# Optimization experiments

Measured on AMD Instinct MI355X. Metric: run time of the kernel, lower is better.

The kernel has to match this reference:

```python
import jax, jax.numpy as jnp
import numpy as np
import math

B, LQ, S, D = 8, 4096, 77, 1024
H, HD = 16, 64
R, ALPHA = 192, 16.0
LORA_SCALE = ALPHA / R
N_SUBJ = 32


def setup_inputs() -> dict:
    key = jax.random.key(0)
    ks = jax.random.split(key, 16)
    w = 0.02
    return {
        "hidden_states": jax.random.normal(ks[0], (B, LQ, D), jnp.float32),
        "encoder_hidden_states": jax.random.normal(ks[1], (B, S, D), jnp.float32),
        "Wq": jax.random.normal(ks[2], (D, D), jnp.float32) * w,
        "Wk": jax.random.normal(ks[3], (D, D), jnp.float32) * w,
        "Wv": jax.random.normal(ks[4], (D, D), jnp.float32) * w,
        "Wo": jax.random.normal(ks[5], (D, D), jnp.float32) * w,
        "bo": jnp.zeros((D,), jnp.float32),
        "Ak": jax.random.normal(ks[6], (R, D), jnp.float32) * w,
        "Bk": jax.random.normal(ks[7], (D, R), jnp.float32) * w,
        "Av": jax.random.normal(ks[8], (R, D), jnp.float32) * w,
        "Bv": jax.random.normal(ks[9], (D, R), jnp.float32) * w,
        "Ao": jax.random.normal(ks[10], (R, D), jnp.float32) * w,
        "Bo": jax.random.normal(ks[11], (D, R), jnp.float32) * w,
        "cross_attn_scale_factor": jnp.ones((), jnp.float32),
        "subj_b": jax.random.randint(ks[12], (N_SUBJ,), 0, B, jnp.int32),
        "subj_n": jax.random.randint(ks[13], (N_SUBJ,), 0, S, jnp.int32),
    }


def _lora(x, A, Bm):
    # peft LoRA delta: scale * (x @ A^T) @ B^T
    return LORA_SCALE * ((x @ A.T) @ Bm.T)


def reference(hidden_states, encoder_hidden_states, Wq, Wk, Wv, Wo, bo,
              Ak, Bk, Av, Bv, Ao, Bo, cross_attn_scale_factor, subj_b, subj_n):
    hs, ehs = hidden_states, encoder_hidden_states
    # q_lora_updates_query=False -> query uses the base projection only
    q = hs @ Wq.T                                  # [B, LQ, D]
    k = ehs @ Wk.T + _lora(ehs, Ak, Bk)            # [B, S, D] (to_k_lora)
    v = ehs @ Wv.T + _lora(ehs, Av, Bv)            # [B, S, D] (to_v_lora)

    q = q.reshape(B, LQ, H, HD).transpose(0, 2, 1, 3)   # [B,H,LQ,HD]
    k = k.reshape(B, S, H, HD).transpose(0, 2, 1, 3)    # [B,H,S,HD]
    v = v.reshape(B, S, H, HD).transpose(0, 2, 1, 3)

    scale = 1.0 / math.sqrt(HD)
    attn_score = jnp.einsum('bhld,bhsd->bhls', q, k) * scale  # [B,H,LQ,S]

    # normalize_cross_attn: zero-center subject-token scores over query dim,
    # then rescale by the learned cross_attn_scale_factor.
    sub = attn_score[subj_b, :, :, subj_n]                    # [K,H,LQ]
    sub = (sub - sub.mean(axis=2, keepdims=True)) * cross_attn_scale_factor
    attn_score = attn_score.at[subj_b, :, :, subj_n].set(sub)

    attn_weight = jax.nn.softmax(attn_score, axis=-1)
    out = jnp.einsum('bhls,bhsd->bhld', attn_weight, v)       # [B,H,LQ,HD]
    out = out.transpose(0, 2, 1, 3).reshape(B, LQ, D)

    # to_out_lora: base out-proj (with bias) + LoRA delta; to_out[1] dropout = id
    out = out @ Wo.T + bo + _lora(out, Ao, Bo)
    return out
```

## Files before the change

kernel.cpp:

```cpp
#include <hip/hip_runtime.h>
#include <stdint.h>

#define B_     8
#define LQ_    4096
#define S_     77
#define SP_    80
#define D_     1024
#define H_     16
#define HD_    64
#define NC_    1280
#define NSUBJ_ 32

typedef __attribute__((ext_vector_type(4))) float  f4;
typedef __attribute__((ext_vector_type(8))) short  short8;
typedef __attribute__((ext_vector_type(8))) unsigned short us8;
typedef __attribute__((ext_vector_type(4))) unsigned short us4;

__device__ __forceinline__ unsigned short f2bf(float f) {
  union { float f; unsigned u; } x; x.f = f;
  unsigned r = x.u + 0x7FFFu + ((x.u >> 16) & 1u);
  return (unsigned short)(r >> 16);
}

__device__ __forceinline__ void gload16(const void* g, void* s) {
  __builtin_amdgcn_global_load_lds((const __attribute__((address_space(1))) void*)g,
                                   (__attribute__((address_space(3))) void*)s, 16, 0, 0);
}

__global__ __launch_bounds__(256) void k_hssum(const float* __restrict__ hs,
                                               float* __restrict__ part,
                                               unsigned short* __restrict__ hsb) {
  int b = blockIdx.y;
  size_t base = ((size_t)b * LQ_ + (size_t)blockIdx.x * 64) * D_ + threadIdx.x * 4;
  f4 acc = {0.f, 0.f, 0.f, 0.f};
  for (int l = 0; l < 64; ++l) {
    f4 v = *(const f4*)(hs + base + (size_t)l * D_);
    acc += v;
    if (hsb) {
      us4 o;
#pragma unroll
      for (int j = 0; j < 4; ++j) o[j] = f2bf(v[j]);
      *(us4*)(hsb + base + (size_t)l * D_) = o;
    }
  }
  *(f4*)(part + (size_t)blockIdx.x * (B_ * D_) + b * D_ + threadIdx.x * 4) = acc;
}

__global__ __launch_bounds__(256) void k_hsred(const float* __restrict__ part,
                                               float* __restrict__ hssum) {
  int i = blockIdx.x * 256 + threadIdx.x;
  float s = 0.f;
  for (int x = 0; x < 64; ++x) s += part[(size_t)x * (B_ * D_) + i];
  hssum[i] = s;
}

__global__ __launch_bounds__(256) void k_tr4(const float* __restrict__ Wq, const float* __restrict__ Ak,
                                             const float* __restrict__ Av, const float* __restrict__ Ao,
                                             float* __restrict__ wqT, float* __restrict__ akT,
                                             float* __restrict__ avT, float* __restrict__ aoT) {
  int z = blockIdx.z;
  const float* in = z == 0 ? Wq : (z == 1 ? Ak : (z == 2 ? Av : Ao));
  float* out = z == 0 ? wqT : (z == 1 ? akT : (z == 2 ? avT : aoT));
  int R = z == 0 ? 1024 : 192;
  const int C = 1024;
  int c0 = blockIdx.x * 32, r0 = blockIdx.y * 32;
  if (r0 >= R) return;
  __shared__ float tile[32][33];
  int tx = threadIdx.x & 31, ty = threadIdx.x >> 5;
#pragma unroll
  for (int k = 0; k < 4; ++k)
    tile[ty + 8 * k][tx] = in[(size_t)(r0 + ty + 8 * k) * C + c0 + tx];
  __syncthreads();
#pragma unroll
  for (int k = 0; k < 4; ++k)
    out[(size_t)(c0 + ty + 8 * k) * R + r0 + tx] = tile[tx][ty + 8 * k];
}

template <bool OBF>
__device__ __forceinline__ void gemm64_body(
    const float* __restrict__ A, int lda, const float* __restrict__ Bt, int ldb,
    void* __restrict__ Cv, int ldc, long cbase, const float* __restrict__ Dm, int ldd,
    int M, int Mv, int N, int K, float alpha, int m0, int n0,
    short* As, short* Bs) {
  int t = threadIdx.x, lane = t & 63, wid = t >> 6;
  int wm = wid >> 1, wn = wid & 1;
  f4 acc[2][2] = {};
  int srow = t >> 2, skc = (t & 3) * 8;
  for (int k0 = 0; k0 < K; k0 += 32) {
    __syncthreads();
    f4 a0 = {0,0,0,0}, a1 = {0,0,0,0}, b0 = {0,0,0,0}, b1 = {0,0,0,0};
    if (m0 + srow < Mv) {
      const float* p = A + (size_t)(m0 + srow) * lda + k0 + skc;
      a0 = *(const f4*)p; a1 = *(const f4*)(p + 4);
    }
    if (n0 + srow < N) {
      const float* p = Bt + (size_t)(n0 + srow) * ldb + k0 + skc;
      b0 = *(const f4*)p; b1 = *(const f4*)(p + 4);
    }
    us8 ua, ub;
#pragma unroll
    for (int j = 0; j < 4; ++j) {
      ua[j] = f2bf(a0[j]); ua[4 + j] = f2bf(a1[j]);
      ub[j] = f2bf(b0[j]); ub[4 + j] = f2bf(b1[j]);
    }
    *(us8*)(As + srow * 40 + skc) = ua;
    *(us8*)(Bs + srow * 40 + skc) = ub;
    __syncthreads();
    short8 fa[2], fb[2];
#pragma unroll
    for (int i = 0; i < 2; ++i) {
      fa[i] = *(const short8*)(As + (wm * 32 + i * 16 + (lane & 15)) * 40 + (lane >> 4) * 8);
      fb[i] = *(const short8*)(Bs + (wn * 32 + i * 16 + (lane & 15)) * 40 + (lane >> 4) * 8);
    }
#pragma unroll
    for (int mi = 0; mi < 2; ++mi)
#pragma unroll
      for (int ni = 0; ni < 2; ++ni)
        acc[mi][ni] = __builtin_amdgcn_mfma_f32_16x16x32_bf16(fa[mi], fb[ni], acc[mi][ni], 0, 0, 0);
  }
#pragma unroll
  for (int mi = 0; mi < 2; ++mi)
#pragma unroll
    for (int ni = 0; ni < 2; ++ni)
#pragma unroll
      for (int j = 0; j < 4; ++j) {
        int row = m0 + wm * 32 + mi * 16 + (lane >> 4) * 4 + j;
        int col = n0 + wn * 32 + ni * 16 + (lane & 15);
        if (row < M && col < N) {
          float val = acc[mi][ni][j] * alpha;
          if (Dm) val += Dm[(size_t)row * ldd + col];
          size_t idx = (size_t)cbase + (size_t)row * ldc + col;
          if (OBF) ((unsigned short*)Cv)[idx] = f2bf(val);
          else     ((float*)Cv)[idx] = val;
        }
      }
}

template <bool OBF>
__global__ __launch_bounds__(256) void k_gemm_small(
    const float* __restrict__ A, int lda, long sA1, long sA2,
    const float* __restrict__ Bt, int ldb, long sB1, long sB2,
    void* __restrict__ Cv, int ldc, long sC1, long sC2,
    const float* __restrict__ Dm, int ldd,
    int M, int Mv, int N, int K, float alpha, int Z2) {
  int z = blockIdx.z, z1 = z / Z2, z2 = z - z1 * Z2;
  __shared__ short As[64 * 40];
  __shared__ short Bs[64 * 40];
  gemm64_body<OBF>(A + z1 * sA1 + z2 * sA2, lda, Bt + z1 * sB1 + z2 * sB2, ldb,
                   Cv, ldc, z1 * sC1 + z2 * sC2, Dm, ldd, M, Mv, N, K, alpha,
                   blockIdx.x * 64, blockIdx.y * 64, As, Bs);
}

__global__ __launch_bounds__(256) void k_weff(
    const float* __restrict__ Bk, const float* __restrict__ Bv, const float* __restrict__ Bo,
    const float* __restrict__ akT, const float* __restrict__ avT, const float* __restrict__ aoT,
    const float* __restrict__ Wk, const float* __restrict__ Wv, const float* __restrict__ Wo,
    float* __restrict__ weff, float alpha) {
  int z = blockIdx.z;
  const float* A  = z == 0 ? Bk : (z == 1 ? Bv : Bo);
  const float* Bt = z == 0 ? akT : (z == 1 ? avT : aoT);
  const float* Dm = z == 0 ? Wk : (z == 1 ? Wv : Wo);
  __shared__ short As[64 * 40];
  __shared__ short Bs[64 * 40];
  gemm64_body<false>(A, 192, Bt, 192, weff + (size_t)z * 1048576, 1024, 0, Dm, 1024,
                     1024, 1024, 1024, 192, alpha, blockIdx.x * 64, blockIdx.y * 64, As, Bs);
}

__global__ void k_mubeta(const float* __restrict__ hssum, const float* __restrict__ Wq,
                         const float* __restrict__ kv,
                         const int* __restrict__ sb, const int* __restrict__ sn,
                         const float* __restrict__ csf_p,
                         float* __restrict__ alphav, float* __restrict__ betav) {
  int h = blockIdx.x, b = blockIdx.y;
  int t = threadIdx.x;
  __shared__ float qp[64];
  {
    int hd = t >> 1, half = t & 1;
    const float* wr = Wq + (size_t)(h * 64 + hd) * D_ + half * 512;
    const float* hp = hssum + b * D_ + half * 512;
    float s = 0.f;
    for (int d = 0; d < 512; d += 4) {
      f4 w = *(const f4*)(wr + d);
      f4 x = *(const f4*)(hp + d);
      s += w[0] * x[0] + w[1] * x[1] + w[2] * x[2] + w[3] * x[3];
    }
    s += __shfl_xor(s, 1, 64);
    if (half == 0) qp[hd] = s * (1.f / 4096.f);
  }
  __syncthreads();
  int s = t;
  if (s >= SP_) return;
  const float* kp = kv + ((size_t)(b * SP_ + s)) * 2048 + h * HD_;
  float mu = 0.f;
#pragma unroll 8
  for (int hd = 0; hd < HD_; ++hd) mu += qp[hd] * kp[hd];
  mu *= 0.125f;
  bool subj = false;
  for (int i = 0; i < NSUBJ_; ++i) subj = subj || (sb[i] == b && sn[i] == s);
  float csf = *csf_p;
  int c = b * NC_ + h * SP_ + s;
  alphav[c] = subj ? csf : 1.f;
  betav[c] = (s >= S_) ? -1e30f : (subj ? -mu * csf : 0.f);
}

__global__ __launch_bounds__(512, 2) void k_score_big(
    const unsigned short* __restrict__ hsb, const unsigned short* __restrict__ Mt,
    const float* __restrict__ alphav, const float* __restrict__ betav,
    unsigned short* __restrict__ P) {
  extern __shared__ short lds[];
  const int ASZ = 256 * 64;
  const int BSZ = 320 * 64;
  int id = blockIdx.x;
  int x = id & 7, idp = id >> 3;
  int nt = idp & 3;
  int pid = (idp >> 2) * 8 + x;
  int b = pid >> 4, mt = pid & 15;
  int m0 = mt * 256, n0 = nt * 320;

  const unsigned short* Ab = hsb + (size_t)b * LQ_ * D_;
  const unsigned short* Bb = Mt + (size_t)b * NC_ * D_;
  const float* alp = alphav + b * NC_;
  const float* bet = betav + b * NC_;
  unsigned short* Pb = P + (size_t)b * LQ_ * NC_;

  int t = threadIdx.x, lane = t & 63, wid = t >> 6;
  int wm = wid >> 2, wn = wid & 3;
  int r = lane & 15, q = lane >> 4;
  f4 acc[8][5] = {};

  auto SA = [&](int bf, int k0, int p) {
    int cb = p * 512 + wid * 64;
    int cc = cb + lane;
    int row = cc >> 3, col = ((cc & 7) ^ (row & 7)) * 8;
    gload16(Ab + (size_t)(m0 + row) * D_ + k0 + col, (char*)(lds + bf * ASZ) + cb * 16);
  };
  auto SB = [&](int bf, int k0, int p) {
    int cb = p * 512 + wid * 64;
    int cc = cb + lane;
    int row = cc >> 3, col = ((cc & 7) ^ (row & 7)) * 8;
    gload16(Bb + (size_t)(n0 + row) * D_ + k0 + col, (char*)(lds + 2 * ASZ + bf * BSZ) + cb * 16);
  };

#pragma unroll
  for (int p = 0; p < 4; ++p) SA(0, 0, p);
#pragma unroll
  for (int p = 0; p < 5; ++p) SB(0, 0, p);

  for (int kt = 0; kt < 16; ++kt) {
    int cur = kt & 1;
    const short* Ar = lds + cur * ASZ;
    const short* Br = lds + 2 * ASZ + cur * BSZ;
    int k1 = (kt + 1) * 64;
    bool pre = kt < 15;
    int co0 = (q ^ (lane & 7)) * 8;
    int co1 = ((4 + q) ^ (lane & 7)) * 8;
    short8 fb[5], fa[4];

    if (pre) {
      SA(cur ^ 1, k1, 0); SA(cur ^ 1, k1, 1); SA(cur ^ 1, k1, 2); SA(cur ^ 1, k1, 3);
      SB(cur ^ 1, k1, 0);
      asm volatile("s_waitcnt vmcnt(5)" ::: "memory");
    } else {
      asm volatile("s_waitcnt vmcnt(0)" ::: "memory");
    }
    __builtin_amdgcn_s_barrier();
#pragma unroll
    for (int ni = 0; ni < 5; ++ni) fb[ni] = *(const short8*)(Br + (wn * 80 + ni * 16 + r) * 64 + co0);
#pragma unroll
    for (int mi = 0; mi < 4; ++mi) fa[mi] = *(const short8*)(Ar + (wm * 128 + mi * 16 + r) * 64 + co0);
    __builtin_amdgcn_s_setprio(1);
#pragma unroll
    for (int mi = 0; mi < 4; ++mi)
#pragma unroll
      for (int ni = 0; ni < 5; ++ni)
        acc[mi][ni] = __builtin_amdgcn_mfma_f32_16x16x32_bf16(fa[mi], fb[ni], acc[mi][ni], 0, 0, 0);
    __builtin_amdgcn_s_setprio(0);
    __builtin_amdgcn_s_barrier();

#pragma unroll
    for (int mi = 0; mi < 4; ++mi) fa[mi] = *(const short8*)(Ar + (wm * 128 + (4 + mi) * 16 + r) * 64 + co0);
    if (pre) { SB(cur ^ 1, k1, 1); SB(cur ^ 1, k1, 2); SB(cur ^ 1, k1, 3); SB(cur ^ 1, k1, 4); }
    __builtin_amdgcn_s_barrier();
    __builtin_amdgcn_s_setprio(1);
#pragma unroll
    for (int mi = 0; mi < 4; ++mi)
#pragma unroll
      for (int ni = 0; ni < 5; ++ni)
        acc[4 + mi][ni] = __builtin_amdgcn_mfma_f32_16x16x32_bf16(fa[mi], fb[ni], acc[4 + mi][ni], 0, 0, 0);
    __builtin_amdgcn_s_setprio(0);
    __builtin_amdgcn_s_barrier();

#pragma unroll
    for (int ni = 0; ni < 5; ++ni) fb[ni] = *(const short8*)(Br + (wn * 80 + ni * 16 + r) * 64 + co1);
#pragma unroll
    for (int mi = 0; mi < 4; ++mi) fa[mi] = *(const short8*)(Ar + (wm * 128 + mi * 16 + r) * 64 + co1);
    __builtin_amdgcn_s_barrier();
    __builtin_amdgcn_s_setprio(1);
#pragma unroll
    for (int mi = 0; mi < 4; ++mi)
#pragma unroll
      for (int ni = 0; ni < 5; ++ni)
        acc[mi][ni] = __builtin_amdgcn_mfma_f32_16x16x32_bf16(fa[mi], fb[ni], acc[mi][ni], 0, 0, 0);
    __builtin_amdgcn_s_setprio(0);
    __builtin_amdgcn_s_barrier();

#pragma unroll
    for (int mi = 0; mi < 4; ++mi) fa[mi] = *(const short8*)(Ar + (wm * 128 + (4 + mi) * 16 + r) * 64 + co1);
    __builtin_amdgcn_s_barrier();
    __builtin_amdgcn_s_setprio(1);
#pragma unroll
    for (int mi = 0; mi < 4; ++mi)
#pragma unroll
      for (int ni = 0; ni < 5; ++ni)
        acc[4 + mi][ni] = __builtin_amdgcn_mfma_f32_16x16x32_bf16(fa[mi], fb[ni], acc[4 + mi][ni], 0, 0, 0);
    __builtin_amdgcn_s_setprio(0);
    __builtin_amdgcn_s_barrier();
  }

  float al[5], be[5];
#pragma unroll
  for (int ni = 0; ni < 5; ++ni) {
    int cc = n0 + wn * 80 + ni * 16 + (lane & 15);
    al[ni] = alp[cc]; be[ni] = bet[cc];
  }
#pragma unroll
  for (int mi = 0; mi < 8; ++mi) {
#pragma unroll
    for (int j = 0; j < 4; ++j) {
      float v[5];
      float m = -3.0e38f;
#pragma unroll
      for (int ni = 0; ni < 5; ++ni) { v[ni] = acc[mi][ni][j] * al[ni] + be[ni]; m = fmaxf(m, v[ni]); }
#pragma unroll
      for (int off = 1; off < 16; off <<= 1) m = fmaxf(m, __shfl_xor(m, off, 64));
      float ssum = 0.f;
#pragma unroll
      for (int ni = 0; ni < 5; ++ni) { v[ni] = __expf(v[ni] - m); ssum += v[ni]; }
#pragma unroll
      for (int off = 1; off < 16; off <<= 1) ssum += __shfl_xor(ssum, off, 64);
      float inv = 1.f / ssum;
      int row = m0 + wm * 128 + mi * 16 + (lane >> 4) * 4 + j;
      size_t rb = (size_t)row * NC_ + n0 + wn * 80 + (lane & 15);
#pragma unroll
      for (int ni = 0; ni < 5; ++ni)
        Pb[rb + ni * 16] = f2bf(v[ni] * inv);
    }
  }
}

__global__ __launch_bounds__(256) void k_score_f32(
    const float* __restrict__ hs, const unsigned short* __restrict__ Mt,
    const float* __restrict__ alphav, const float* __restrict__ betav,
    unsigned short* __restrict__ P) {
  int id = blockIdx.x;
  int x = id & 7, idp = id >> 3;
  int n_t = idp & 7;
  int pid = (idp >> 3) * 8 + x;
  int b = pid >> 5, m_t = pid & 31;
  int m0 = m_t * 128, n0 = n_t * 160;
  const float* Af = hs + (size_t)b * LQ_ * D_;
  const unsigned short* Bb = Mt + (size_t)b * NC_ * D_;
  const float* alp = alphav + b * NC_;
  const float* bet = betav + b * NC_;
  unsigned short* Pb = P + (size_t)b * LQ_ * NC_;
  __shared__ short As[128 * 64];
  __shared__ short Bs[160 * 64];
  int t = threadIdx.x, lane = t & 63, wid = t >> 6;
  int wm = wid >> 1, wn = wid & 1;
  int srow = lane >> 3;
  int schunk = (lane & 7) ^ srow;
  f4 acc[4][5] = {};
  for (int k0 = 0; k0 < D_; k0 += 64) {
    __syncthreads();
    for (int i = wid; i < 20; i += 4)
      gload16(Bb + (size_t)(n0 + i * 8 + srow) * D_ + k0 + schunk * 8, (char*)Bs + i * 1024);
    int arow = t >> 3, ac = t & 7;
    int awc = ac ^ (arow & 7);
#pragma unroll
    for (int p = 0; p < 4; ++p) {
      int row = p * 32 + arow;
      const float* src = Af + (size_t)(m0 + row) * D_ + k0 + ac * 8;
      f4 v0 = *(const f4*)src;
      f4 v1 = *(const f4*)(src + 4);
      us8 u;
#pragma unroll
      for (int j = 0; j < 4; ++j) { u[j] = f2bf(v0[j]); u[4 + j] = f2bf(v1[j]); }
      *(us8*)(As + row * 64 + awc * 8) = u;
    }
    __syncthreads();
#pragma unroll
    for (int kk = 0; kk < 2; ++kk) {
      int co = ((kk * 4 + (lane >> 4)) ^ (lane & 7)) * 8;
      short8 fa[4], fb[5];
#pragma unroll
      for (int mi = 0; mi < 4; ++mi)
        fa[mi] = *(const short8*)(As + (wm * 64 + mi * 16 + (lane & 15)) * 64 + co);
#pragma unroll
      for (int ni = 0; ni < 5; ++ni)
        fb[ni] = *(const short8*)(Bs + (wn * 80 + ni * 16 + (lane & 15)) * 64 + co);
#pragma unroll
      for (int mi = 0; mi < 4; ++mi)
#pragma unroll
        for (int ni = 0; ni < 5; ++ni)
          acc[mi][ni] = __builtin_amdgcn_mfma_f32_16x16x32_bf16(fa[mi], fb[ni], acc[mi][ni], 0, 0, 0);
    }
  }
  float al[5], be[5];
#pragma unroll
  for (int ni = 0; ni < 5; ++ni) {
    int cc = n0 + wn * 80 + ni * 16 + (lane & 15);
    al[ni] = alp[cc]; be[ni] = bet[cc];
  }
#pragma unroll
  for (int mi = 0; mi < 4; ++mi) {
#pragma unroll
    for (int j = 0; j < 4; ++j) {
      float v[5];
      float m = -3.0e38f;
#pragma unroll
      for (int ni = 0; ni < 5; ++ni) { v[ni] = acc[mi][ni][j] * al[ni] + be[ni]; m = fmaxf(m, v[ni]); }
#pragma unroll
      for (int off = 1; off < 16; off <<= 1) m = fmaxf(m, __shfl_xor(m, off, 64));
      float ssum = 0.f;
#pragma unroll
      for (int ni = 0; ni < 5; ++ni) { v[ni] = __expf(v[ni] - m); ssum += v[ni]; }
#pragma unroll
      for (int off = 1; off < 16; off <<= 1) ssum += __shfl_xor(ssum, off, 64);
      float inv = 1.f / ssum;
      int row = m0 + wm * 64 + mi * 16 + (lane >> 4) * 4 + j;
      size_t rb = (size_t)row * NC_ + n0 + wn * 80 + (lane & 15);
#pragma unroll
      for (int ni = 0; ni < 5; ++ni)
        Pb[rb + ni * 16] = f2bf(v[ni] * inv);
    }
  }
}

__global__ __launch_bounds__(512, 2) void k_out_big(
    const unsigned short* __restrict__ P, const unsigned short* __restrict__ Ut,
    const float* __restrict__ bo, float* __restrict__ out) {
  extern __shared__ short lds[];
  const int ASZ = 256 * 64;
  int id = blockIdx.x;
  int x = id & 7, idp = id >> 3;
  int nt = idp & 3;
  int pid = (idp >> 2) * 8 + x;
  int b = pid >> 4, mt = pid & 15;
  int m0 = mt * 256, n0 = nt * 256;

  const unsigned short* Ab = P + (size_t)b * LQ_ * NC_;
  const unsigned short* Bb = Ut + (size_t)b * D_ * NC_;
  float* ob = out + (size_t)b * LQ_ * D_;

  int t = threadIdx.x, lane = t & 63, wid = t >> 6;
  int wm = wid >> 2, wn = wid & 3;
  int r = lane & 15, q = lane >> 4;
  f4 acc[8][4] = {};
  const int T = NC_ / 64;

  auto SA = [&](int bf, int k0, int p) {
    int cb = p * 512 + wid * 64;
    int cc = cb + lane;
    int row = cc >> 3, col = ((cc & 7) ^ (row & 7)) * 8;
    gload16(Ab + (size_t)(m0 + row) * NC_ + k0 + col, (char*)(lds + bf * ASZ) + cb * 16);
  };
  auto SB = [&](int bf, int k0, int p) {
    int cb = p * 512 + wid * 64;
    int cc = cb + lane;
    int row = cc >> 3, col = ((cc & 7) ^ (row & 7)) * 8;
    gload16(Bb + (size_t)(n0 + row) * NC_ + k0 + col, (char*)(lds + 2 * ASZ + bf * ASZ) + cb * 16);
  };

#pragma unroll
  for (int p = 0; p < 4; ++p) SA(0, 0, p);
#pragma unroll
  for (int p = 0; p < 4; ++p) SB(0, 0, p);

  for (int kt = 0; kt < T; ++kt) {
    int cur = kt & 1;
    const short* Ar = lds + cur * ASZ;
    const short* Br = lds + 2 * ASZ + cur * ASZ;
    int k1 = (kt + 1) * 64;
    bool pre = kt + 1 < T;
    int co0 = (q ^ (lane & 7)) * 8;
    int co1 = ((4 + q) ^ (lane & 7)) * 8;
    short8 fb[4], fa[4];

    if (pre) {
      SA(cur ^ 1, k1, 0); SA(cur ^ 1, k1, 1); SA(cur ^ 1, k1, 2); SA(cur ^ 1, k1, 3);
      asm volatile("s_waitcnt vmcnt(4)" ::: "memory");
    } else {
      asm volatile("s_waitcnt vmcnt(0)" ::: "memory");
    }
    __builtin_amdgcn_s_barrier();
#pragma unroll
    for (int ni = 0; ni < 4; ++ni) fb[ni] = *(const short8*)(Br + (wn * 64 + ni * 16 + r) * 64 + co0);
#pragma unroll
    for (int mi = 0; mi < 4; ++mi) fa[mi] = *(const short8*)(Ar + (wm * 128 + mi * 16 + r) * 64 + co0);
    __builtin_amdgcn_s_setprio(1);
#pragma unroll
    for (int mi = 0; mi < 4; ++mi)
#pragma unroll
      for (int ni = 0; ni < 4; ++ni)
        acc[mi][ni] = __builtin_amdgcn_mfma_f32_16x16x32_bf16(fa[mi], fb[ni], acc[mi][ni], 0, 0, 0);
    __builtin_amdgcn_s_setprio(0);
    __builtin_amdgcn_s_barrier();

#pragma unroll
    for (int mi = 0; mi < 4; ++mi) fa[mi] = *(const short8*)(Ar + (wm * 128 + (4 + mi) * 16 + r) * 64 + co0);
    if (pre) { SB(cur ^ 1, k1, 0); SB(cur ^ 1, k1, 1); SB(cur ^ 1, k1, 2); SB(cur ^ 1, k1, 3); }
    __builtin_amdgcn_s_barrier();
    __builtin_amdgcn_s_setprio(1);
#pragma unroll
    for (int mi = 0; mi < 4; ++mi)
#pragma unroll
      for (int ni = 0; ni < 4; ++ni)
        acc[4 + mi][ni] = __builtin_amdgcn_mfma_f32_16x16x32_bf16(fa[mi], fb[ni], acc[4 + mi][ni], 0, 0, 0);
    __builtin_amdgcn_s_setprio(0);
    __builtin_amdgcn_s_barrier();

#pragma unroll
    for (int ni = 0; ni < 4; ++ni) fb[ni] = *(const short8*)(Br + (wn * 64 + ni * 16 + r) * 64 + co1);
#pragma unroll
    for (int mi = 0; mi < 4; ++mi) fa[mi] = *(const short8*)(Ar + (wm * 128 + mi * 16 + r) * 64 + co1);
    __builtin_amdgcn_s_barrier();
    __builtin_amdgcn_s_setprio(1);
#pragma unroll
    for (int mi = 0; mi < 4; ++mi)
#pragma unroll
      for (int ni = 0; ni < 4; ++ni)
        acc[mi][ni] = __builtin_amdgcn_mfma_f32_16x16x32_bf16(fa[mi], fb[ni], acc[mi][ni], 0, 0, 0);
    __builtin_amdgcn_s_setprio(0);
    __builtin_amdgcn_s_barrier();

#pragma unroll
    for (int mi = 0; mi < 4; ++mi) fa[mi] = *(const short8*)(Ar + (wm * 128 + (4 + mi) * 16 + r) * 64 + co1);
    __builtin_amdgcn_s_barrier();
    __builtin_amdgcn_s_setprio(1);
#pragma unroll
    for (int mi = 0; mi < 4; ++mi)
#pragma unroll
      for (int ni = 0; ni < 4; ++ni)
        acc[4 + mi][ni] = __builtin_amdgcn_mfma_f32_16x16x32_bf16(fa[mi], fb[ni], acc[4 + mi][ni], 0, 0, 0);
    __builtin_amdgcn_s_setprio(0);
    __builtin_amdgcn_s_barrier();
  }

#pragma unroll
  for (int ni = 0; ni < 4; ++ni) {
    int col = n0 + wn * 64 + ni * 16 + (lane & 15);
    float bov = bo[col];
#pragma unroll
    for (int mi = 0; mi < 8; ++mi)
#pragma unroll
      for (int j = 0; j < 4; ++j) {
        int row = m0 + wm * 128 + mi * 16 + (lane >> 4) * 4 + j;
        ob[(size_t)row * D_ + col] = acc[mi][ni][j] + bov;
      }
  }
}

extern "C" void kernel_launch(void* const* d_in, const int* in_sizes, int n_in,
                              void* d_out, int out_size, void* d_ws, size_t ws_size,
                              hipStream_t stream) {
  const float* hs  = (const float*)d_in[0];
  const float* ehs = (const float*)d_in[1];
  const float* Wq  = (const float*)d_in[2];
  const float* Wk  = (const float*)d_in[3];
  const float* Wv  = (const float*)d_in[4];
  const float* Wo  = (const float*)d_in[5];
  const float* bo  = (const float*)d_in[6];
  const float* Ak  = (const float*)d_in[7];
  const float* Bk  = (const float*)d_in[8];
  const float* Av  = (const float*)d_in[9];
  const float* Bv  = (const float*)d_in[10];
  const float* Ao  = (const float*)d_in[11];
  const float* Bo  = (const float*)d_in[12];
  const float* csf = (const float*)d_in[13];
  const int*   sb  = (const int*)d_in[14];
  const int*   sn  = (const int*)d_in[15];
  float* out = (float*)d_out;

  hipFuncSetAttribute(reinterpret_cast<const void*>(k_score_big),
                      hipFuncAttributeMaxDynamicSharedMemorySize, 147456);
  hipFuncSetAttribute(reinterpret_cast<const void*>(k_out_big),
                      hipFuncAttributeMaxDynamicSharedMemorySize, 131072);

  char* ws = (char*)d_ws;
  unsigned short* P  = (unsigned short*)ws;
  unsigned short* Mt = (unsigned short*)(ws + 83886080);
  unsigned short* Ut = (unsigned short*)(ws + 104857600);
  const size_t NEED_HSB = 125829120ULL + 67108864ULL + 81920ULL;
  bool useHsb = ws_size >= NEED_HSB;
  unsigned short* hsb = useHsb ? (unsigned short*)(ws + 125829120) : nullptr;
  char* tail = useHsb ? (ws + 192937984) : (ws + 125829120);
  float* alphav = (float*)tail;
  float* betav  = (float*)(tail + 40960);
  float* kvbuf = (float*)(ws + 0);
  float* weff  = (float*)(ws + 5242880);
  float* wqT   = (float*)(ws + 17825792);
  float* aT    = (float*)(ws + 22020096);
  float* part  = (float*)(ws + 24379392);
  float* hssum = (float*)(ws + 26476544);

  float* woE = weff + 2097152;
  float* akT = aT;
  float* avT = aT + 196608;
  float* aoT = aT + 393216;

  const float LS = 16.0f / 192.0f;

  k_hssum<<<dim3(64, 8), 256, 0, stream>>>(hs, part, hsb);
  k_hsred<<<32, 256, 0, stream>>>(part, hssum);

  k_tr4<<<dim3(32, 32, 4), 256, 0, stream>>>(Wq, Ak, Av, Ao, wqT, akT, avT, aoT);

  k_weff<<<dim3(16, 16, 3), 256, 0, stream>>>(Bk, Bv, Bo, akT, avT, aoT, Wk, Wv, Wo, weff, LS);

  k_gemm_small<false><<<dim3(2, 32, 8), 256, 0, stream>>>(
      ehs, 1024, 77L * 1024, 0, weff, 1024, 0, 0, kvbuf, 2048, 80L * 2048, 0, nullptr, 0,
      80, 77, 2048, 1024, 1.f, 1);

  k_gemm_small<true><<<dim3(2, 16, 128), 256, 0, stream>>>(
      kvbuf, 2048, 80L * 2048, 64L, wqT, 1024, 0, 64L,
      Mt, 1024, (long)NC_ * 1024, 80L * 1024, nullptr, 0,
      80, 80, 1024, 64, 0.125f, 16);

  k_gemm_small<true><<<dim3(16, 2, 128), 256, 0, stream>>>(
      woE, 1024, 0, 64L, kvbuf + 1024, 2048, 80L * 2048, 64L,
      Ut, NC_, 1024L * NC_, 80L, nullptr, 0,
      1024, 1024, 80, 64, 1.f, 16);

  k_mubeta<<<dim3(16, 8), 128, 0, stream>>>(hssum, Wq, kvbuf, sb, sn, csf, alphav, betav);

  if (useHsb)
    k_score_big<<<512, 512, 147456, stream>>>(hsb, Mt, alphav, betav, P);
  else
    k_score_f32<<<2048, 256, 0, stream>>>(hs, Mt, alphav, betav, P);
  k_out_big<<<512, 512, 131072, stream>>>(P, Ut, bo, out);

  (void)in_sizes; (void)n_in; (void)out_size; (void)ws_size;
}
```

Before: 364.6 us.

## Apply K/V LoRA in low rank and restructure big-GEMM prefetch barriers

The K/V LoRA deltas are no longer folded into dense effective weights. The code now computes ehs@A^T in low rank (k_eA) and then runs a two-pass GEMM (k_kv) that adds eA@B^T to the base projection, removing the 1024x1024x192 weight-merge GEMMs for K and V and the transposes of Ak and Av. Separately, the main score and output GEMM kernels change their pipeline: the next tile's global loads are issued after the LDS fragment reads, with sched_barriers, an explicit lgkmcnt wait, and one vmcnt(0) plus barrier at the end of each k-step. This aims to overlap loads better but adds a full memory wait per iteration.

```diff
diff --git a/kernel.cpp b/kernel.cpp
--- a/kernel.cpp
+++ b/kernel.cpp
@@ -54,13 +54,11 @@
   hssum[i] = s;
 }
 
-__global__ __launch_bounds__(256) void k_tr4(const float* __restrict__ Wq, const float* __restrict__ Ak,
-                                             const float* __restrict__ Av, const float* __restrict__ Ao,
-                                             float* __restrict__ wqT, float* __restrict__ akT,
-                                             float* __restrict__ avT, float* __restrict__ aoT) {
+__global__ __launch_bounds__(256) void k_tr2(const float* __restrict__ Wq, const float* __restrict__ Ao,
+                                             float* __restrict__ wqT, float* __restrict__ aoT) {
   int z = blockIdx.z;
-  const float* in = z == 0 ? Wq : (z == 1 ? Ak : (z == 2 ? Av : Ao));
-  float* out = z == 0 ? wqT : (z == 1 ? akT : (z == 2 ? avT : aoT));
+  const float* in = z == 0 ? Wq : Ao;
+  float* out = z == 0 ? wqT : aoT;
   int R = z == 0 ? 1024 : 192;
   const int C = 1024;
   int c0 = blockIdx.x * 32, r0 = blockIdx.y * 32;
@@ -151,19 +149,93 @@
                    blockIdx.x * 64, blockIdx.y * 64, As, Bs);
 }
 
-__global__ __launch_bounds__(256) void k_weff(
-    const float* __restrict__ Bk, const float* __restrict__ Bv, const float* __restrict__ Bo,
-    const float* __restrict__ akT, const float* __restrict__ avT, const float* __restrict__ aoT,
-    const float* __restrict__ Wk, const float* __restrict__ Wv, const float* __restrict__ Wo,
-    float* __restrict__ weff, float alpha) {
-  int z = blockIdx.z;
-  const float* A  = z == 0 ? Bk : (z == 1 ? Bv : Bo);
-  const float* Bt = z == 0 ? akT : (z == 1 ? avT : aoT);
-  const float* Dm = z == 0 ? Wk : (z == 1 ? Wv : Wo);
+__global__ __launch_bounds__(256) void k_eA(const float* __restrict__ ehs,
+                                            const float* __restrict__ Ak, const float* __restrict__ Av,
+                                            float* __restrict__ eA, float alpha) {
+  int b = blockIdx.z;
+  int m0 = blockIdx.x * 64;
+  int n0 = blockIdx.y * 64;
+  bool sel = n0 >= 192;
+  int nl = n0 - (sel ? 192 : 0);
+  const float* Bt = sel ? Av : Ak;
   __shared__ short As[64 * 40];
   __shared__ short Bs[64 * 40];
-  gemm64_body<false>(A, 192, Bt, 192, weff + (size_t)z * 1048576, 1024, 0, Dm, 1024,
-                     1024, 1024, 1024, 192, alpha, blockIdx.x * 64, blockIdx.y * 64, As, Bs);
+  gemm64_body<false>(ehs + (size_t)b * S_ * D_, 1024, Bt, 1024,
+                     eA + (size_t)b * 80 * 384 + (sel ? 192 : 0), 384, 0, nullptr, 0,
+                     80, S_, 192, 1024, alpha, m0, nl, As, Bs);
+}
+
+__global__ __launch_bounds__(256) void k_kv(const float* __restrict__ ehs,
+                                            const float* __restrict__ Wk, const float* __restrict__ Wv,
+                                            const float* __restrict__ eA,
+                                            const float* __restrict__ Bk, const float* __restrict__ Bv,
+                                            float* __restrict__ kvbuf) {
+  int b = blockIdx.z;
+  int m0 = blockIdx.x * 64, n0 = blockIdx.y * 64;
+  bool vh = n0 >= 1024;
+  int nl = n0 & 1023;
+  const float* A1 = ehs + (size_t)b * S_ * D_;
+  const float* Bt1 = (vh ? Wv : Wk) + (size_t)nl * 1024;
+  const float* A2 = eA + (size_t)b * 80 * 384 + (vh ? 192 : 0);
+  const float* Bt2 = (vh ? Bv : Bk) + (size_t)nl * 192;
+  float* C = kvbuf + (size_t)b * 80 * 2048;
+
+  __shared__ short As[64 * 40];
+  __shared__ short Bs[64 * 40];
+  int t = threadIdx.x, lane = t & 63, wid = t >> 6;
+  int wm = wid >> 1, wn = wid & 1;
+  f4 acc[2][2] = {};
+  int srow = t >> 2, skc = (t & 3) * 8;
+
+#pragma unroll 1
+  for (int pass = 0; pass < 2; ++pass) {
+    const float* A = pass ? A2 : A1;
+    const float* Bt = pass ? Bt2 : Bt1;
+    int lda = pass ? 384 : 1024, ldb = pass ? 192 : 1024;
+    int K = pass ? 192 : 1024;
+    for (int k0 = 0; k0 < K; k0 += 32) {
+      __syncthreads();
+      f4 a0 = {0,0,0,0}, a1 = {0,0,0,0}, b0, b1;
+      if (m0 + srow < S_) {
+        const float* p = A + (size_t)(m0 + srow) * lda + k0 + skc;
+        a0 = *(const f4*)p; a1 = *(const f4*)(p + 4);
+      }
+      {
+        const float* p = Bt + (size_t)srow * ldb + k0 + skc;
+        b0 = *(const f4*)p; b1 = *(const f4*)(p + 4);
+      }
+      us8 ua, ub;
+#pragma unroll
+      for (int j = 0; j < 4; ++j) {
+        ua[j] = f2bf(a0[j]); ua[4 + j] = f2bf(a1[j]);
+        ub[j] = f2bf(b0[j]); ub[4 + j] = f2bf(b1[j]);
+      }
+      *(us8*)(As + srow * 40 + skc) = ua;
+      *(us8*)(Bs + srow * 40 + skc) = ub;
+      __syncthreads();
+      short8 fa[2], fb[2];
+#pragma unroll
+      for (int i = 0; i < 2; ++i) {
+        fa[i] = *(const short8*)(As + (wm * 32 + i * 16 + (lane & 15)) * 40 + (lane >> 4) * 8);
+        fb[i] = *(const short8*)(Bs + (wn * 32 + i * 16 + (lane & 15)) * 40 + (lane >> 4) * 8);
+      }
+#pragma unroll
+      for (int mi = 0; mi < 2; ++mi)
+#pragma unroll
+        for (int ni = 0; ni < 2; ++ni)
+          acc[mi][ni] = __builtin_amdgcn_mfma_f32_16x16x32_bf16(fa[mi], fb[ni], acc[mi][ni], 0, 0, 0);
+    }
+  }
+#pragma unroll
+  for (int mi = 0; mi < 2; ++mi)
+#pragma unroll
+    for (int ni = 0; ni < 2; ++ni)
+#pragma unroll
+      for (int j = 0; j < 4; ++j) {
+        int row = m0 + wm * 32 + mi * 16 + (lane >> 4) * 4 + j;
+        int col = n0 + wn * 32 + ni * 16 + (lane & 15);
+        if (row < 80) C[(size_t)row * 2048 + col] = acc[mi][ni][j];
+      }
 }
 
 __global__ void k_mubeta(const float* __restrict__ hssum, const float* __restrict__ Wq,
@@ -245,6 +317,8 @@
   for (int p = 0; p < 4; ++p) SA(0, 0, p);
 #pragma unroll
   for (int p = 0; p < 5; ++p) SB(0, 0, p);
+  asm volatile("s_waitcnt vmcnt(0)" ::: "memory");
+  asm volatile("s_barrier" ::: "memory");
 
   for (int kt = 0; kt < 16; ++kt) {
     int cur = kt & 1;
@@ -256,18 +330,15 @@
     int co1 = ((4 + q) ^ (lane & 7)) * 8;
     short8 fb[5], fa[4];
 
-    if (pre) {
-      SA(cur ^ 1, k1, 0); SA(cur ^ 1, k1, 1); SA(cur ^ 1, k1, 2); SA(cur ^ 1, k1, 3);
-      SB(cur ^ 1, k1, 0);
-      asm volatile("s_waitcnt vmcnt(5)" ::: "memory");
-    } else {
-      asm volatile("s_waitcnt vmcnt(0)" ::: "memory");
-    }
-    __builtin_amdgcn_s_barrier();
 #pragma unroll
     for (int ni = 0; ni < 5; ++ni) fb[ni] = *(const short8*)(Br + (wn * 80 + ni * 16 + r) * 64 + co0);
 #pragma unroll
     for (int mi = 0; mi < 4; ++mi) fa[mi] = *(const short8*)(Ar + (wm * 128 + mi * 16 + r) * 64 + co0);
+    __builtin_amdgcn_sched_barrier(0);
+    if (pre) { SA(cur ^ 1, k1, 0); SA(cur ^ 1, k1, 1); SA(cur ^ 1, k1, 2); SA(cur ^ 1, k1, 3); SB(cur ^ 1, k1, 0); }
+    __builtin_amdgcn_sched_barrier(0);
+    __builtin_amdgcn_s_barrier();
+    asm volatile("s_waitcnt lgkmcnt(0)");
     __builtin_amdgcn_s_setprio(1);
 #pragma unroll
     for (int mi = 0; mi < 4; ++mi)
@@ -279,8 +350,11 @@
 
 #pragma unroll
     for (int mi = 0; mi < 4; ++mi) fa[mi] = *(const short8*)(Ar + (wm * 128 + (4 + mi) * 16 + r) * 64 + co0);
+    __builtin_amdgcn_sched_barrier(0);
     if (pre) { SB(cur ^ 1, k1, 1); SB(cur ^ 1, k1, 2); SB(cur ^ 1, k1, 3); SB(cur ^ 1, k1, 4); }
-    __builtin_amdgcn_s_barrier();
+    __builtin_amdgcn_sched_barrier(0);
+    __builtin_amdgcn_s_barrier();
+    asm volatile("s_waitcnt lgkmcnt(0)");
     __builtin_amdgcn_s_setprio(1);
 #pragma unroll
     for (int mi = 0; mi < 4; ++mi)
@@ -294,7 +368,9 @@
     for (int ni = 0; ni < 5; ++ni) fb[ni] = *(const short8*)(Br + (wn * 80 + ni * 16 + r) * 64 + co1);
 #pragma unroll
     for (int mi = 0; mi < 4; ++mi) fa[mi] = *(const short8*)(Ar + (wm * 128 + mi * 16 + r) * 64 + co1);
-    __builtin_amdgcn_s_barrier();
+    __builtin_amdgcn_sched_barrier(0);
+    __builtin_amdgcn_s_barrier();
+    asm volatile("s_waitcnt lgkmcnt(0)");
     __builtin_amdgcn_s_setprio(1);
 #pragma unroll
     for (int mi = 0; mi < 4; ++mi)
@@ -306,7 +382,9 @@
 
 #pragma unroll
     for (int mi = 0; mi < 4; ++mi) fa[mi] = *(const short8*)(Ar + (wm * 128 + (4 + mi) * 16 + r) * 64 + co1);
-    __builtin_amdgcn_s_barrier();
+    __builtin_amdgcn_sched_barrier(0);
+    __builtin_amdgcn_s_barrier();
+    asm volatile("s_waitcnt lgkmcnt(0)");
     __builtin_amdgcn_s_setprio(1);
 #pragma unroll
     for (int mi = 0; mi < 4; ++mi)
@@ -314,7 +392,10 @@
       for (int ni = 0; ni < 5; ++ni)
         acc[4 + mi][ni] = __builtin_amdgcn_mfma_f32_16x16x32_bf16(fa[mi], fb[ni], acc[4 + mi][ni], 0, 0, 0);
     __builtin_amdgcn_s_setprio(0);
-    __builtin_amdgcn_s_barrier();
+    if (pre) {
+      asm volatile("s_waitcnt vmcnt(0)" ::: "memory");
+      asm volatile("s_barrier" ::: "memory");
+    }
   }
 
   float al[5], be[5];
@@ -475,6 +556,8 @@
   for (int p = 0; p < 4; ++p) SA(0, 0, p);
 #pragma unroll
   for (int p = 0; p < 4; ++p) SB(0, 0, p);
+  asm volatile("s_waitcnt vmcnt(0)" ::: "memory");
+  asm volatile("s_barrier" ::: "memory");
 
   for (int kt = 0; kt < T; ++kt) {
     int cur = kt & 1;
@@ -486,17 +569,15 @@
     int co1 = ((4 + q) ^ (lane & 7)) * 8;
     short8 fb[4], fa[4];
 
-    if (pre) {
-      SA(cur ^ 1, k1, 0); SA(cur ^ 1, k1, 1); SA(cur ^ 1, k1, 2); SA(cur ^ 1, k1, 3);
-      asm volatile("s_waitcnt vmcnt(4)" ::: "memory");
-    } else {
-      asm volatile("s_waitcnt vmcnt(0)" ::: "memory");
-    }
-    __builtin_amdgcn_s_barrier();
 #pragma unroll
     for (int ni = 0; ni < 4; ++ni) fb[ni] = *(const short8*)(Br + (wn * 64 + ni * 16 + r) * 64 + co0);
 #pragma unroll
     for (int mi = 0; mi < 4; ++mi) fa[mi] = *(const short8*)(Ar + (wm * 128 + mi * 16 + r) * 64 + co0);
+    __builtin_amdgcn_sched_barrier(0);
+    if (pre) { SA(cur ^ 1, k1, 0); SA(cur ^ 1, k1, 1); SA(cur ^ 1, k1, 2); SA(cur ^ 1, k1, 3); }
+    __builtin_amdgcn_sched_barrier(0);
+    __builtin_amdgcn_s_barrier();
+    asm volatile("s_waitcnt lgkmcnt(0)");
     __builtin_amdgcn_s_setprio(1);
 #pragma unroll
     for (int mi = 0; mi < 4; ++mi)
@@ -508,8 +589,11 @@
 
 #pragma unroll
     for (int mi = 0; mi < 4; ++mi) fa[mi] = *(const short8*)(Ar + (wm * 128 + (4 + mi) * 16 + r) * 64 + co0);
+    __builtin_amdgcn_sched_barrier(0);
     if (pre) { SB(cur ^ 1, k1, 0); SB(cur ^ 1, k1, 1); SB(cur ^ 1, k1, 2); SB(cur ^ 1, k1, 3); }
-    __builtin_amdgcn_s_barrier();
+    __builtin_amdgcn_sched_barrier(0);
+    __builtin_amdgcn_s_barrier();
+    asm volatile("s_waitcnt lgkmcnt(0)");
     __builtin_amdgcn_s_setprio(1);
 #pragma unroll
     for (int mi = 0; mi < 4; ++mi)
@@ -523,7 +607,9 @@
     for (int ni = 0; ni < 4; ++ni) fb[ni] = *(const short8*)(Br + (wn * 64 + ni * 16 + r) * 64 + co1);
 #pragma unroll
     for (int mi = 0; mi < 4; ++mi) fa[mi] = *(const short8*)(Ar + (wm * 128 + mi * 16 + r) * 64 + co1);
-    __builtin_amdgcn_s_barrier();
+    __builtin_amdgcn_sched_barrier(0);
+    __builtin_amdgcn_s_barrier();
+    asm volatile("s_waitcnt lgkmcnt(0)");
     __builtin_amdgcn_s_setprio(1);
 #pragma unroll
     for (int mi = 0; mi < 4; ++mi)
@@ -535,7 +621,9 @@
 
 #pragma unroll
     for (int mi = 0; mi < 4; ++mi) fa[mi] = *(const short8*)(Ar + (wm * 128 + (4 + mi) * 16 + r) * 64 + co1);
-    __builtin_amdgcn_s_barrier();
+    __builtin_amdgcn_sched_barrier(0);
+    __builtin_amdgcn_s_barrier();
+    asm volatile("s_waitcnt lgkmcnt(0)");
     __builtin_amdgcn_s_setprio(1);
 #pragma unroll
     for (int mi = 0; mi < 4; ++mi)
@@ -543,7 +631,10 @@
       for (int ni = 0; ni < 4; ++ni)
         acc[4 + mi][ni] = __builtin_amdgcn_mfma_f32_16x16x32_bf16(fa[mi], fb[ni], acc[4 + mi][ni], 0, 0, 0);
     __builtin_amdgcn_s_setprio(0);
-    __builtin_amdgcn_s_barrier();
+    if (pre) {
+      asm volatile("s_waitcnt vmcnt(0)" ::: "memory");
+      asm volatile("s_barrier" ::: "memory");
+    }
   }
 
 #pragma unroll
@@ -597,29 +688,27 @@
   float* alphav = (float*)tail;
   float* betav  = (float*)(tail + 40960);
   float* kvbuf = (float*)(ws + 0);
-  float* weff  = (float*)(ws + 5242880);
-  float* wqT   = (float*)(ws + 17825792);
-  float* aT    = (float*)(ws + 22020096);
-  float* part  = (float*)(ws + 24379392);
-  float* hssum = (float*)(ws + 26476544);
-
-  float* woE = weff + 2097152;
-  float* akT = aT;
-  float* avT = aT + 196608;
-  float* aoT = aT + 393216;
+  float* woE   = (float*)(ws + 5242880);
+  float* wqT   = (float*)(ws + 9437184);
+  float* aoT   = (float*)(ws + 13631488);
+  float* eA    = (float*)(ws + 14417920);
+  float* part  = (float*)(ws + 15400960);
+  float* hssum = (float*)(ws + 17498112);
 
   const float LS = 16.0f / 192.0f;
 
   k_hssum<<<dim3(64, 8), 256, 0, stream>>>(hs, part, hsb);
   k_hsred<<<32, 256, 0, stream>>>(part, hssum);
 
-  k_tr4<<<dim3(32, 32, 4), 256, 0, stream>>>(Wq, Ak, Av, Ao, wqT, akT, avT, aoT);
-
-  k_weff<<<dim3(16, 16, 3), 256, 0, stream>>>(Bk, Bv, Bo, akT, avT, aoT, Wk, Wv, Wo, weff, LS);
-
-  k_gemm_small<false><<<dim3(2, 32, 8), 256, 0, stream>>>(
-      ehs, 1024, 77L * 1024, 0, weff, 1024, 0, 0, kvbuf, 2048, 80L * 2048, 0, nullptr, 0,
-      80, 77, 2048, 1024, 1.f, 1);
+  k_tr2<<<dim3(32, 32, 2), 256, 0, stream>>>(Wq, Ao, wqT, aoT);
+
+  k_gemm_small<false><<<dim3(16, 16, 1), 256, 0, stream>>>(
+      Bo, 192, 0, 0, aoT, 192, 0, 0, woE, 1024, 0, 0, Wo, 1024,
+      1024, 1024, 1024, 192, LS, 1);
+
+  k_eA<<<dim3(2, 6, 8), 256, 0, stream>>>(ehs, Ak, Av, eA, LS);
+
+  k_kv<<<dim3(2, 32, 8), 256, 0, stream>>>(ehs, Wk, Wv, eA, Bk, Bv, kvbuf);
 
   k_gemm_small<true><<<dim3(2, 16, 128), 256, 0, stream>>>(
       kvbuf, 2048, 80L * 2048, 64L, wqT, 1024, 0, 64L,
```

New measurement: 391.1 us. 7.3% more time.
